# Optimization experiments

Hardware: AMD Instinct MI355X
Metric: run time of the kernel (lower is better)

The kernel has to match this reference:

```python
import jax, jax.numpy as jnp
import numpy as np
import math

B, C, DH = 2048, 64, 512
CAP_VOCAB = 11  # max(core_capacities)+1
DIST_VOCAB = 3


def setup_inputs() -> dict:
    key = jax.random.key(0)
    ks = jax.random.split(key, 12)
    inp = {
        "Ht_C": jax.random.normal(ks[0], (B, C, DH), jnp.float32),
        "core_capacities": jax.random.randint(ks[1], (B, C), 0, CAP_VOCAB),
        "distances": jax.random.randint(ks[2], (B, C), 0, DIST_VOCAB),
        "H_X": jax.random.normal(ks[3], (B, DH), jnp.float32),
        "Ht_S": jax.random.normal(ks[4], (B, DH), jnp.float32),
        "Eq_Q": jax.random.normal(ks[5], (B, DH), jnp.float32),
        "double": jax.random.randint(ks[6], (B,), 0, 2).astype(bool),
        # learned parameters (nn.Embedding tables and bias-free Linear weights, [out,in])
        "cap_emb": jax.random.normal(ks[7], (CAP_VOCAB, DH), jnp.float32) * 0.02,
        "dist_emb": jax.random.normal(ks[8], (DIST_VOCAB, DH), jnp.float32) * 0.02,
        "W_q": jax.random.normal(ks[9], (DH, 3 * DH), jnp.float32) * (1.0 / math.sqrt(3 * DH)),
        "W_k": jax.random.normal(ks[10], (DH, DH), jnp.float32) * (1.0 / math.sqrt(DH)),
        "W_v": jax.random.normal(ks[11], (DH, DH), jnp.float32) * (1.0 / math.sqrt(DH)),
    }
    return inp


def reference(Ht_C, core_capacities, distances, H_X, Ht_S, Eq_Q, double,
              cap_emb, dist_emb, W_q, W_k, W_v):
    scale = 1.0 / math.sqrt(Ht_C.shape[-1])  # 1/sqrt(d_H), slice_emb_size == d_H
    # dynamic core embeddings G_{t,q}^{(C)}: [B,C,dH]
    G = Ht_C + cap_emb[core_capacities] + dist_emb[distances]
    # context and projections
    context = jnp.concatenate([H_X, Ht_S, Eq_Q], axis=-1)          # [B,3dH]
    Q = context @ W_q.T                                            # [B,dH]
    K = jnp.einsum('bcd,ed->bce', G, W_k)                          # [B,C,dH]
    V = jnp.einsum('bcd,ed->bce', G, W_v)                          # [B,C,dH]
    # glimpse attention over cores
    attn_logits = jnp.einsum('bcd,bd->bc', K, Q) * scale           # [B,C]
    attn_weights = jax.nn.softmax(attn_logits, axis=-1)            # softmax over cores
    glimpse = jnp.einsum('bc,bcd->bd', attn_weights, V)            # [B,dH]
    # pointer logits + capacity mask
    u = jnp.einsum('bcd,bd->bc', K, glimpse) * scale               # [B,C]
    need = jnp.where(double[:, None], 2, 1)                        # [B,1]
    invalid = core_capacities < need                               # [B,C]
    u = jnp.where(invalid, -jnp.inf, u)
    return jax.nn.softmax(u, axis=-1)                              # [B,C]
```

## Files before the change

### kernel.cpp

```cpp
#include <hip/hip_runtime.h>
#include <math.h>

#define DH 512
#define CC 64
#define NB 2048
#define SCALE 0.044194173824159216f

__device__ __forceinline__ float wsum(float v) {
#pragma unroll
  for (int off = 32; off; off >>= 1) v += __shfl_xor(v, off, 64);
  return v;
}

__global__ __launch_bounds__(128) void pre_kernel(const float* __restrict__ Wq,
                                                  const float* __restrict__ Wv,
                                                  const float* __restrict__ Wk,
                                                  float* __restrict__ Aout,
                                                  float* __restrict__ Mout,
                                                  const unsigned char* __restrict__ dbl,
                                                  int* __restrict__ need) {
  const int bx = blockIdx.x;
  const int t = threadIdx.x;
  if (bx == 256) {
    __shared__ int flagNZ, flagFP;
    if (t == 0) { flagNZ = 0; flagFP = 0; }
    __syncthreads();
    int nz = 0, fp = 0;
    for (int i = t; i < NB; i += 128) {
      if (i & 3) {
        unsigned char v = dbl[i];
        nz |= (v != 0);
        fp |= (v == 0x3f) | (v == 0x80);
      }
    }
    if (nz) atomicOr(&flagNZ, 1);
    if (fp) atomicOr(&flagFP, 1);
    __syncthreads();
    const int isFP = flagFP, isByte = flagNZ && !flagFP;
    for (int i = t; i < NB; i += 128) {
      int v;
      if (isFP)        v = (((const float*)dbl)[i] != 0.0f);
      else if (isByte) v = (dbl[i] != 0);
      else             v = (((const int*)dbl)[i] != 0);
      need[i] = v ? 2 : 1;
    }
    return;
  }
  __shared__ float As[16][64];
  __shared__ float Bs[16][64];
  const int mt = bx >> 3, nt = bx & 7;
  const int m0 = mt * 64, n0 = nt * 64;
  const bool isQ = (m0 < 1536);
  const float* Acol = isQ ? (Wq + m0) : (Wv + (m0 - 1536));
  const int lda = isQ ? 1536 : 512;
  float* Cout = isQ ? (Aout + (size_t)m0 * 512) : (Mout + (size_t)(m0 - 1536) * 512);
  const int lr = t >> 3;
  const int lc = (t & 7) << 3;
  const int tx = t & 15, ty = t >> 4;

  float4 ra0, ra1, rb0, rb1;
  ra0 = *(const float4*)&Acol[(size_t)lr * lda + lc];
  ra1 = *(const float4*)&Acol[(size_t)lr * lda + lc + 4];
  rb0 = *(const float4*)&Wk[(size_t)lr * 512 + n0 + lc];
  rb1 = *(const float4*)&Wk[(size_t)lr * 512 + n0 + lc + 4];
  float acc[8][4] = {};
  for (int k0 = 0; k0 < 512; k0 += 16) {
    __syncthreads();
    *(float4*)&As[lr][lc] = ra0;
    *(float4*)&As[lr][lc + 4] = ra1;
    *(float4*)&Bs[lr][lc] = rb0;
    *(float4*)&Bs[lr][lc + 4] = rb1;
    __syncthreads();
    if (k0 + 16 < 512) {
      const int kn = k0 + 16 + lr;
      ra0 = *(const float4*)&Acol[(size_t)kn * lda + lc];
      ra1 = *(const float4*)&Acol[(size_t)kn * lda + lc + 4];
      rb0 = *(const float4*)&Wk[(size_t)kn * 512 + n0 + lc];
      rb1 = *(const float4*)&Wk[(size_t)kn * 512 + n0 + lc + 4];
    }
#pragma unroll
    for (int k = 0; k < 16; ++k) {
      float4 a0 = *(float4*)&As[k][ty << 3];
      float4 a1 = *(float4*)&As[k][(ty << 3) + 4];
      float4 b  = *(float4*)&Bs[k][tx << 2];
      float av[8] = {a0.x, a0.y, a0.z, a0.w, a1.x, a1.y, a1.z, a1.w};
      float bv[4] = {b.x, b.y, b.z, b.w};
#pragma unroll
      for (int i = 0; i < 8; ++i)
#pragma unroll
        for (int j = 0; j < 4; ++j) acc[i][j] = fmaf(av[i], bv[j], acc[i][j]);
    }
  }
#pragma unroll
  for (int i = 0; i < 8; ++i) {
    float4 o = {acc[i][0], acc[i][1], acc[i][2], acc[i][3]};
    *(float4*)&Cout[(size_t)((ty << 3) + i) * 512 + n0 + (tx << 2)] = o;
  }
}

#define AS_STR 132

__global__ __launch_bounds__(256) void gemm_nn2p(const float* __restrict__ A0,
                                                 const float* __restrict__ A1,
                                                 const float* __restrict__ A2,
                                                 const float* __restrict__ B,
                                                 float* __restrict__ Cp,
                                                 int kchunk) {
  __shared__ float As[16 * AS_STR];
  __shared__ float Bs[16 * 64];
  const int t = threadIdx.x;
  const int m0 = blockIdx.x * 128, n0 = blockIdx.y * 64;
  const int kbeg = blockIdx.z * kchunk, kend = kbeg + kchunk;
  float* C = Cp + (size_t)blockIdx.z * (NB * DH);
  const int tx = t & 15, ty = t >> 4;
  const int ar0 = t >> 2;
  const int ak4 = (t & 3) << 2;
  const int bk = t >> 4, bn4 = (t & 15) << 2;

  float4 ra0, ra1, rb;
  {
    const float* base = (kbeg < 512) ? A0 : ((kbeg < 1024) ? A1 : A2);
    const int kk = kbeg & 511;
    ra0 = *(const float4*)&base[(size_t)(m0 + ar0) * 512 + kk + ak4];
    ra1 = *(const float4*)&base[(size_t)(m0 + ar0 + 64) * 512 + kk + ak4];
    rb  = *(const float4*)&B[(size_t)(kbeg + bk) * 512 + n0 + bn4];
  }
  float acc[8][4] = {};
  for (int k0 = kbeg; k0 < kend; k0 += 16) {
    __syncthreads();
    As[(ak4 + 0) * AS_STR + ar0] = ra0.x;
    As[(ak4 + 1) * AS_STR + ar0] = ra0.y;
    As[(ak4 + 2) * AS_STR + ar0] = ra0.z;
    As[(ak4 + 3) * AS_STR + ar0] = ra0.w;
    As[(ak4 + 0) * AS_STR + ar0 + 64] = ra1.x;
    As[(ak4 + 1) * AS_STR + ar0 + 64] = ra1.y;
    As[(ak4 + 2) * AS_STR + ar0 + 64] = ra1.z;
    As[(ak4 + 3) * AS_STR + ar0 + 64] = ra1.w;
    *(float4*)&Bs[bk * 64 + bn4] = rb;
    __syncthreads();
    if (k0 + 16 < kend) {
      const int kn = k0 + 16;
      const float* base = (kn < 512) ? A0 : ((kn < 1024) ? A1 : A2);
      const int kk = kn & 511;
      ra0 = *(const float4*)&base[(size_t)(m0 + ar0) * 512 + kk + ak4];
      ra1 = *(const float4*)&base[(size_t)(m0 + ar0 + 64) * 512 + kk + ak4];
      rb  = *(const float4*)&B[(size_t)(kn + bk) * 512 + n0 + bn4];
    }
#pragma unroll
    for (int k = 0; k < 16; ++k) {
      float4 a0 = *(float4*)&As[k * AS_STR + (ty << 3)];
      float4 a1 = *(float4*)&As[k * AS_STR + (ty << 3) + 4];
      float4 b  = *(float4*)&Bs[k * 64 + (tx << 2)];
      float av[8] = {a0.x, a0.y, a0.z, a0.w, a1.x, a1.y, a1.z, a1.w};
      float bv[4] = {b.x, b.y, b.z, b.w};
#pragma unroll
      for (int i = 0; i < 8; ++i)
#pragma unroll
        for (int j = 0; j < 4; ++j) acc[i][j] = fmaf(av[i], bv[j], acc[i][j]);
    }
  }
#pragma unroll
  for (int i = 0; i < 8; ++i) {
    float4 o = {acc[i][0], acc[i][1], acc[i][2], acc[i][3]};
    *(float4*)&C[(size_t)(m0 + (ty << 3) + i) * 512 + n0 + (tx << 2)] = o;
  }
}

__global__ __launch_bounds__(256) void pass1_kernel(const float* __restrict__ HtC,
                                                    const int* __restrict__ caps,
                                                    const int* __restrict__ dists,
                                                    const float* __restrict__ Qkp,
                                                    const float* __restrict__ cap_emb,
                                                    const float* __restrict__ dist_emb,
                                                    float* __restrict__ Gw) {
  const int b = blockIdx.x;
  const int t = threadIdx.x;
  const int wv = t >> 6, ln = t & 63;
  __shared__ float qk[DH];
  __shared__ float capQ[11], distQ[3];
  __shared__ float capE[11], distE[3];
  __shared__ float ec[CC];
  __shared__ float accs[4][DH];
  __shared__ float lsum_s;
  if (t < 11) capE[t] = 0.f;
  if (t < 3) distE[t] = 0.f;
  {
    float q0 = 0.f, q1 = 0.f;
#pragma unroll
    for (int z = 0; z < 4; ++z) {
      q0 += Qkp[(size_t)z * NB * DH + (size_t)b * DH + t];
      q1 += Qkp[(size_t)z * NB * DH + (size_t)b * DH + 256 + t];
    }
    qk[t] = q0;
    qk[t + 256] = q1;
  }
  __syncthreads();
#pragma unroll
  for (int r = 0; r < 3; ++r) {
    int v = wv + (r << 2);
    if (v < 11) {
      float s = 0.f;
#pragma unroll
      for (int j = 0; j < 8; ++j) s = fmaf(cap_emb[v * DH + ln + (j << 6)], qk[ln + (j << 6)], s);
      s = wsum(s);
      if (ln == 0) capQ[v] = s;
    }
  }
  if (wv < 3) {
    float s = 0.f;
#pragma unroll
    for (int j = 0; j < 8; ++j) s = fmaf(dist_emb[wv * DH + ln + (j << 6)], qk[ln + (j << 6)], s);
    s = wsum(s);
    if (ln == 0) distQ[wv] = s;
  }
  __syncthreads();
  const float4* qk4 = (const float4*)qk;
  float4 q1 = qk4[ln];
  float4 q2 = qk4[64 + ln];
  const float* hb = HtC + (size_t)b * CC * DH;
  float a0 = 0.f, a1 = 0.f, a2 = 0.f, a3 = 0.f, a4 = 0.f, a5 = 0.f, a6 = 0.f, a7 = 0.f;
#pragma unroll 4
  for (int i = 0; i < 16; ++i) {
    int c = (wv << 4) + i;
    const float4* h4 = (const float4*)(hb + (size_t)c * DH);
    float4 h1 = h4[ln];
    float4 h2 = h4[64 + ln];
    float s = h1.x * q1.x + h1.y * q1.y + h1.z * q1.z + h1.w * q1.w +
              h2.x * q2.x + h2.y * q2.y + h2.z * q2.z + h2.w * q2.w;
    s = wsum(s);
    float logit = SCALE * (s + capQ[caps[b * CC + c]] + distQ[dists[b * CC + c]]);
    float e = __expf(logit);
    if (ln == 0) ec[c] = e;
    a0 = fmaf(e, h1.x, a0); a1 = fmaf(e, h1.y, a1);
    a2 = fmaf(e, h1.z, a2); a3 = fmaf(e, h1.w, a3);
    a4 = fmaf(e, h2.x, a4); a5 = fmaf(e, h2.y, a5);
    a6 = fmaf(e, h2.z, a6); a7 = fmaf(e, h2.w, a7);
  }
  {
    int d0 = ln << 2;
    accs[wv][d0 + 0] = a0; accs[wv][d0 + 1] = a1;
    accs[wv][d0 + 2] = a2; accs[wv][d0 + 3] = a3;
    accs[wv][256 + d0 + 0] = a4; accs[wv][256 + d0 + 1] = a5;
    accs[wv][256 + d0 + 2] = a6; accs[wv][256 + d0 + 3] = a7;
  }
  __syncthreads();
  if (t < CC) {
    float e = ec[t];
    float l = wsum(e);
    if (t == 0) lsum_s = l;
    atomicAdd(&capE[caps[b * CC + t]], e);
    atomicAdd(&distE[dists[b * CC + t]], e);
  }
  __syncthreads();
  const float rinv = 1.0f / lsum_s;
#pragma unroll
  for (int dd = 0; dd < 2; ++dd) {
    int d = t + (dd << 8);
    float g = accs[0][d] + accs[1][d] + accs[2][d] + accs[3][d];
#pragma unroll
    for (int v = 0; v < 11; ++v) g = fmaf(capE[v], cap_emb[v * DH + d], g);
#pragma unroll
    for (int v = 0; v < 3; ++v) g = fmaf(distE[v], dist_emb[v * DH + d], g);
    Gw[(size_t)b * DH + d] = g * rinv;
  }
}

__global__ __launch_bounds__(256) void pass2_kernel(const float* __restrict__ HtC,
                                                    const int* __restrict__ caps,
                                                    const int* __restrict__ dists,
                                                    const float* __restrict__ Gkp,
                                                    const float* __restrict__ cap_emb,
                                                    const float* __restrict__ dist_emb,
                                                    const int* __restrict__ need,
                                                    float* __restrict__ out) {
  const int b = NB - 1 - blockIdx.x;
  const int t = threadIdx.x;
  const int wv = t >> 6, ln = t & 63;
  __shared__ float gk[DH];
  __shared__ float capG[11], distG[3];
  __shared__ float ulog[CC];
  {
    float g0 = Gkp[(size_t)b * DH + t] + Gkp[(size_t)NB * DH + (size_t)b * DH + t];
    float g1 = Gkp[(size_t)b * DH + 256 + t] + Gkp[(size_t)NB * DH + (size_t)b * DH + 256 + t];
    gk[t] = g0;
    gk[t + 256] = g1;
  }
  __syncthreads();
#pragma unroll
  for (int r = 0; r < 3; ++r) {
    int v = wv + (r << 2);
    if (v < 11) {
      float s = 0.f;
#pragma unroll
      for (int j = 0; j < 8; ++j) s = fmaf(cap_emb[v * DH + ln + (j << 6)], gk[ln + (j << 6)], s);
      s = wsum(s);
      if (ln == 0) capG[v] = s;
    }
  }
  if (wv < 3) {
    float s = 0.f;
#pragma unroll
    for (int j = 0; j < 8; ++j) s = fmaf(dist_emb[wv * DH + ln + (j << 6)], gk[ln + (j << 6)], s);
    s = wsum(s);
    if (ln == 0) distG[wv] = s;
  }
  __syncthreads();
  const float4* gk4 = (const float4*)gk;
  float4 q1 = gk4[ln];
  float4 q2 = gk4[64 + ln];
  const float* hb = HtC + (size_t)b * CC * DH;
#pragma unroll 4
  for (int i = 0; i < 16; ++i) {
    int c = (wv << 4) + i;
    const float4* h4 = (const float4*)(hb + (size_t)c * DH);
    float4 h1 = h4[ln];
    float4 h2 = h4[64 + ln];
    float s = h1.x * q1.x + h1.y * q1.y + h1.z * q1.z + h1.w * q1.w +
              h2.x * q2.x + h2.y * q2.y + h2.z * q2.z + h2.w * q2.w;
    s = wsum(s);
    if (ln == 0)
      ulog[c] = SCALE * (s + capG[caps[b * CC + c]] + distG[dists[b * CC + c]]);
  }
  __syncthreads();
  if (t < CC) {
    int nb = need[b];
    float x = ulog[t];
    if (caps[b * CC + t] < nb) x = -INFINITY;
    float m = x;
#pragma unroll
    for (int off = 32; off; off >>= 1) m = fmaxf(m, __shfl_xor(m, off, 64));
    float e = __expf(x - m);
    float ssum = wsum(e);
    out[(size_t)b * CC + t] = e / ssum;
  }
}

extern "C" void kernel_launch(void* const* d_in, const int* in_sizes, int n_in,
                              void* d_out, int out_size, void* d_ws, size_t ws_size,
                              hipStream_t stream) {
  const float* HtC      = (const float*)d_in[0];
  const int* caps       = (const int*)d_in[1];
  const int* dists      = (const int*)d_in[2];
  const float* H_X      = (const float*)d_in[3];
  const float* Ht_S     = (const float*)d_in[4];
  const float* Eq_Q     = (const float*)d_in[5];
  const unsigned char* dbl = (const unsigned char*)d_in[6];
  const float* cap_emb  = (const float*)d_in[7];
  const float* dist_emb = (const float*)d_in[8];
  const float* W_q      = (const float*)d_in[9];
  const float* W_k      = (const float*)d_in[10];
  const float* W_v      = (const float*)d_in[11];
  float* out = (float*)d_out;

  float* ws     = (float*)d_ws;
  float* wsA    = ws;
  float* wsM    = wsA + 1536 * 512;
  float* wsQkp  = wsM + 512 * 512;
  float* wsGw   = wsQkp + 4 * 2048 * 512;
  float* wsGkp  = wsGw + 2048 * 512;
  int* wsNeed   = (int*)(wsGkp + 2 * 2048 * 512);

  pre_kernel<<<257, 128, 0, stream>>>(W_q, W_v, W_k, wsA, wsM, dbl, wsNeed);
  gemm_nn2p<<<dim3(16, 8, 4), 256, 0, stream>>>(H_X, Ht_S, Eq_Q, wsA, wsQkp, 384);
  pass1_kernel<<<NB, 256, 0, stream>>>(HtC, caps, dists, wsQkp, cap_emb, dist_emb, wsGw);
  gemm_nn2p<<<dim3(16, 8, 2), 256, 0, stream>>>(wsGw, wsGw, wsGw, wsM, wsGkp, 256);
  pass2_kernel<<<NB, 256, 0, stream>>>(HtC, caps, dists, wsGkp, cap_emb, dist_emb, wsNeed, out);
}
```

Before: 527.9 us.

## Fuse pass1, G·M projection GEMM and pass2 into one kernel per batch pair

Replaces the pass1 kernel, the second GEMM and the pass2 kernel with one fused kernel, where each block handles two batch rows. The block computes the glimpse-weighted G, multiplies it by M in-block while streaming M once per pair of rows, then re-reads Ht_C to produce the masked pointer softmax. This removes two launches and the Gw/Gkp workspace round trips, and the second read of Ht_C comes soon after the first, so it may hit in cache. In exchange, each block re-reads the full 512x512 M matrix (1 MB per block, shared by only two rows), uses more shared memory, and the grid is half as large.

```diff
diff --git a/kernel.cpp b/kernel.cpp
--- a/kernel.cpp
+++ b/kernel.cpp
@@ -166,172 +166,208 @@
   }
 }
 
-__global__ __launch_bounds__(256) void pass1_kernel(const float* __restrict__ HtC,
-                                                    const int* __restrict__ caps,
-                                                    const int* __restrict__ dists,
-                                                    const float* __restrict__ Qkp,
-                                                    const float* __restrict__ cap_emb,
-                                                    const float* __restrict__ dist_emb,
-                                                    float* __restrict__ Gw) {
-  const int b = blockIdx.x;
+__global__ __launch_bounds__(256, 4) void fused_kernel(const float* __restrict__ HtC,
+                                                       const int* __restrict__ caps,
+                                                       const int* __restrict__ dists,
+                                                       const float* __restrict__ Qkp,
+                                                       const float* __restrict__ Mm,
+                                                       const float* __restrict__ cap_emb,
+                                                       const float* __restrict__ dist_emb,
+                                                       const int* __restrict__ need,
+                                                       float* __restrict__ out) {
   const int t = threadIdx.x;
   const int wv = t >> 6, ln = t & 63;
-  __shared__ float qk[DH];
-  __shared__ float capQ[11], distQ[3];
+  const int b0 = blockIdx.x << 1;
+
+  __shared__ float qk[2][DH];
+  __shared__ float Gws[2][DH];
+  __shared__ float gks[2][DH];
+  __shared__ float gkp[2][2][DH];
+  __shared__ float accs[4][DH];
+  __shared__ float ec[CC];
+  __shared__ float capQ[2][11], distQ[2][3];
   __shared__ float capE[11], distE[3];
-  __shared__ float ec[CC];
-  __shared__ float accs[4][DH];
+  __shared__ float capG[2][11], distG[2][3];
   __shared__ float lsum_s;
-  if (t < 11) capE[t] = 0.f;
-  if (t < 3) distE[t] = 0.f;
+
+#pragma unroll
+  for (int h = 0; h < 2; ++h) {
+    const size_t bo = (size_t)(b0 + h) * DH;
+    float q0 = 0.f, q1 = 0.f;
+#pragma unroll
+    for (int z = 0; z < 4; ++z) {
+      q0 += Qkp[(size_t)z * NB * DH + bo + t];
+      q1 += Qkp[(size_t)z * NB * DH + bo + 256 + t];
+    }
+    qk[h][t] = q0;
+    qk[h][t + 256] = q1;
+  }
+  __syncthreads();
+
+#pragma unroll
+  for (int h = 0; h < 2; ++h) {
+#pragma unroll
+    for (int r = 0; r < 3; ++r) {
+      int v = wv + (r << 2);
+      if (v < 11) {
+        float s = 0.f;
+#pragma unroll
+        for (int j = 0; j < 8; ++j) s = fmaf(cap_emb[v * DH + ln + (j << 6)], qk[h][ln + (j << 6)], s);
+        s = wsum(s);
+        if (ln == 0) capQ[h][v] = s;
+      }
+    }
+    if (wv < 3) {
+      float s = 0.f;
+#pragma unroll
+      for (int j = 0; j < 8; ++j) s = fmaf(dist_emb[wv * DH + ln + (j << 6)], qk[h][ln + (j << 6)], s);
+      s = wsum(s);
+      if (ln == 0) distQ[h][wv] = s;
+    }
+  }
+
+  for (int h = 0; h < 2; ++h) {
+    const int b = b0 + h;
+    if (t < 11) capE[t] = 0.f;
+    if (t < 3) distE[t] = 0.f;
+    __syncthreads();
+    const float4* qk4 = (const float4*)qk[h];
+    float4 q1 = qk4[ln];
+    float4 q2 = qk4[64 + ln];
+    const float* hb = HtC + (size_t)b * CC * DH;
+    float a0 = 0.f, a1 = 0.f, a2 = 0.f, a3 = 0.f, a4 = 0.f, a5 = 0.f, a6 = 0.f, a7 = 0.f;
+#pragma unroll 4
+    for (int i = 0; i < 16; ++i) {
+      int c = (wv << 4) + i;
+      const float4* h4 = (const float4*)(hb + (size_t)c * DH);
+      float4 h1 = h4[ln];
+      float4 h2 = h4[64 + ln];
+      float s = h1.x * q1.x + h1.y * q1.y + h1.z * q1.z + h1.w * q1.w +
+                h2.x * q2.x + h2.y * q2.y + h2.z * q2.z + h2.w * q2.w;
+      s = wsum(s);
+      float logit = SCALE * (s + capQ[h][caps[b * CC + c]] + distQ[h][dists[b * CC + c]]);
+      float e = __expf(logit);
+      if (ln == 0) ec[c] = e;
+      a0 = fmaf(e, h1.x, a0); a1 = fmaf(e, h1.y, a1);
+      a2 = fmaf(e, h1.z, a2); a3 = fmaf(e, h1.w, a3);
+      a4 = fmaf(e, h2.x, a4); a5 = fmaf(e, h2.y, a5);
+      a6 = fmaf(e, h2.z, a6); a7 = fmaf(e, h2.w, a7);
+    }
+    {
+      int d0 = ln << 2;
+      accs[wv][d0 + 0] = a0; accs[wv][d0 + 1] = a1;
+      accs[wv][d0 + 2] = a2; accs[wv][d0 + 3] = a3;
+      accs[wv][256 + d0 + 0] = a4; accs[wv][256 + d0 + 1] = a5;
+      accs[wv][256 + d0 + 2] = a6; accs[wv][256 + d0 + 3] = a7;
+    }
+    __syncthreads();
+    if (t < CC) {
+      float e = ec[t];
+      float l = wsum(e);
+      if (t == 0) lsum_s = l;
+      atomicAdd(&capE[caps[b * CC + t]], e);
+      atomicAdd(&distE[dists[b * CC + t]], e);
+    }
+    __syncthreads();
+    const float rinv = 1.0f / lsum_s;
+#pragma unroll
+    for (int dd = 0; dd < 2; ++dd) {
+      int d = t + (dd << 8);
+      float g = accs[0][d] + accs[1][d] + accs[2][d] + accs[3][d];
+#pragma unroll
+      for (int v = 0; v < 11; ++v) g = fmaf(capE[v], cap_emb[v * DH + d], g);
+#pragma unroll
+      for (int v = 0; v < 3; ++v) g = fmaf(distE[v], dist_emb[v * DH + d], g);
+      Gws[h][d] = g * rinv;
+    }
+    __syncthreads();
+  }
+
   {
-    float q0 = 0.f, q1 = 0.f;
-#pragma unroll
-    for (int z = 0; z < 4; ++z) {
-      q0 += Qkp[(size_t)z * NB * DH + (size_t)b * DH + t];
-      q1 += Qkp[(size_t)z * NB * DH + (size_t)b * DH + 256 + t];
-    }
-    qk[t] = q0;
-    qk[t + 256] = q1;
+    const int e4 = (t & 127) << 2;
+    const int half = t >> 7;
+    const float* Mp = Mm + (size_t)(half << 8) * DH + e4;
+    const float* g0p = &Gws[0][half << 8];
+    const float* g1p = &Gws[1][half << 8];
+    float s00 = 0.f, s01 = 0.f, s02 = 0.f, s03 = 0.f;
+    float s10 = 0.f, s11 = 0.f, s12 = 0.f, s13 = 0.f;
+#pragma unroll 8
+    for (int d = 0; d < 256; ++d) {
+      float4 m4 = *(const float4*)&Mp[(size_t)d * DH];
+      float g0 = g0p[d];
+      float g1 = g1p[d];
+      s00 = fmaf(g0, m4.x, s00); s01 = fmaf(g0, m4.y, s01);
+      s02 = fmaf(g0, m4.z, s02); s03 = fmaf(g0, m4.w, s03);
+      s10 = fmaf(g1, m4.x, s10); s11 = fmaf(g1, m4.y, s11);
+      s12 = fmaf(g1, m4.z, s12); s13 = fmaf(g1, m4.w, s13);
+    }
+    gkp[half][0][e4 + 0] = s00; gkp[half][0][e4 + 1] = s01;
+    gkp[half][0][e4 + 2] = s02; gkp[half][0][e4 + 3] = s03;
+    gkp[half][1][e4 + 0] = s10; gkp[half][1][e4 + 1] = s11;
+    gkp[half][1][e4 + 2] = s12; gkp[half][1][e4 + 3] = s13;
   }
   __syncthreads();
 #pragma unroll
-  for (int r = 0; r < 3; ++r) {
-    int v = wv + (r << 2);
-    if (v < 11) {
+  for (int h = 0; h < 2; ++h) {
+    gks[h][t] = gkp[0][h][t] + gkp[1][h][t];
+    gks[h][t + 256] = gkp[0][h][t + 256] + gkp[1][h][t + 256];
+  }
+  __syncthreads();
+
+#pragma unroll
+  for (int h = 0; h < 2; ++h) {
+#pragma unroll
+    for (int r = 0; r < 3; ++r) {
+      int v = wv + (r << 2);
+      if (v < 11) {
+        float s = 0.f;
+#pragma unroll
+        for (int j = 0; j < 8; ++j) s = fmaf(cap_emb[v * DH + ln + (j << 6)], gks[h][ln + (j << 6)], s);
+        s = wsum(s);
+        if (ln == 0) capG[h][v] = s;
+      }
+    }
+    if (wv < 3) {
       float s = 0.f;
 #pragma unroll
-      for (int j = 0; j < 8; ++j) s = fmaf(cap_emb[v * DH + ln + (j << 6)], qk[ln + (j << 6)], s);
+      for (int j = 0; j < 8; ++j) s = fmaf(dist_emb[wv * DH + ln + (j << 6)], gks[h][ln + (j << 6)], s);
       s = wsum(s);
-      if (ln == 0) capQ[v] = s;
-    }
-  }
-  if (wv < 3) {
-    float s = 0.f;
-#pragma unroll
-    for (int j = 0; j < 8; ++j) s = fmaf(dist_emb[wv * DH + ln + (j << 6)], qk[ln + (j << 6)], s);
-    s = wsum(s);
-    if (ln == 0) distQ[wv] = s;
+      if (ln == 0) distG[h][wv] = s;
+    }
   }
   __syncthreads();
-  const float4* qk4 = (const float4*)qk;
-  float4 q1 = qk4[ln];
-  float4 q2 = qk4[64 + ln];
-  const float* hb = HtC + (size_t)b * CC * DH;
-  float a0 = 0.f, a1 = 0.f, a2 = 0.f, a3 = 0.f, a4 = 0.f, a5 = 0.f, a6 = 0.f, a7 = 0.f;
+
+  for (int h = 1; h >= 0; --h) {
+    const int b = b0 + h;
+    const float4* gk4 = (const float4*)gks[h];
+    float4 q1 = gk4[ln];
+    float4 q2 = gk4[64 + ln];
+    const float* hb = HtC + (size_t)b * CC * DH;
 #pragma unroll 4
-  for (int i = 0; i < 16; ++i) {
-    int c = (wv << 4) + i;
-    const float4* h4 = (const float4*)(hb + (size_t)c * DH);
-    float4 h1 = h4[ln];
-    float4 h2 = h4[64 + ln];
-    float s = h1.x * q1.x + h1.y * q1.y + h1.z * q1.z + h1.w * q1.w +
-              h2.x * q2.x + h2.y * q2.y + h2.z * q2.z + h2.w * q2.w;
-    s = wsum(s);
-    float logit = SCALE * (s + capQ[caps[b * CC + c]] + distQ[dists[b * CC + c]]);
-    float e = __expf(logit);
-    if (ln == 0) ec[c] = e;
-    a0 = fmaf(e, h1.x, a0); a1 = fmaf(e, h1.y, a1);
-    a2 = fmaf(e, h1.z, a2); a3 = fmaf(e, h1.w, a3);
-    a4 = fmaf(e, h2.x, a4); a5 = fmaf(e, h2.y, a5);
-    a6 = fmaf(e, h2.z, a6); a7 = fmaf(e, h2.w, a7);
-  }
-  {
-    int d0 = ln << 2;
-    accs[wv][d0 + 0] = a0; accs[wv][d0 + 1] = a1;
-    accs[wv][d0 + 2] = a2; accs[wv][d0 + 3] = a3;
-    accs[wv][256 + d0 + 0] = a4; accs[wv][256 + d0 + 1] = a5;
-    accs[wv][256 + d0 + 2] = a6; accs[wv][256 + d0 + 3] = a7;
-  }
-  __syncthreads();
-  if (t < CC) {
-    float e = ec[t];
-    float l = wsum(e);
-    if (t == 0) lsum_s = l;
-    atomicAdd(&capE[caps[b * CC + t]], e);
-    atomicAdd(&distE[dists[b * CC + t]], e);
-  }
-  __syncthreads();
-  const float rinv = 1.0f / lsum_s;
-#pragma unroll
-  for (int dd = 0; dd < 2; ++dd) {
-    int d = t + (dd << 8);
-    float g = accs[0][d] + accs[1][d] + accs[2][d] + accs[3][d];
-#pragma unroll
-    for (int v = 0; v < 11; ++v) g = fmaf(capE[v], cap_emb[v * DH + d], g);
-#pragma unroll
-    for (int v = 0; v < 3; ++v) g = fmaf(distE[v], dist_emb[v * DH + d], g);
-    Gw[(size_t)b * DH + d] = g * rinv;
-  }
-}
-
-__global__ __launch_bounds__(256) void pass2_kernel(const float* __restrict__ HtC,
-                                                    const int* __restrict__ caps,
-                                                    const int* __restrict__ dists,
-                                                    const float* __restrict__ Gkp,
-                                                    const float* __restrict__ cap_emb,
-                                                    const float* __restrict__ dist_emb,
-                                                    const int* __restrict__ need,
-                                                    float* __restrict__ out) {
-  const int b = NB - 1 - blockIdx.x;
-  const int t = threadIdx.x;
-  const int wv = t >> 6, ln = t & 63;
-  __shared__ float gk[DH];
-  __shared__ float capG[11], distG[3];
-  __shared__ float ulog[CC];
-  {
-    float g0 = Gkp[(size_t)b * DH + t] + Gkp[(size_t)NB * DH + (size_t)b * DH + t];
-    float g1 = Gkp[(size_t)b * DH + 256 + t] + Gkp[(size_t)NB * DH + (size_t)b * DH + 256 + t];
-    gk[t] = g0;
-    gk[t + 256] = g1;
-  }
-  __syncthreads();
-#pragma unroll
-  for (int r = 0; r < 3; ++r) {
-    int v = wv + (r << 2);
-    if (v < 11) {
-      float s = 0.f;
-#pragma unroll
-      for (int j = 0; j < 8; ++j) s = fmaf(cap_emb[v * DH + ln + (j << 6)], gk[ln + (j << 6)], s);
+    for (int i = 0; i < 16; ++i) {
+      int c = (wv << 4) + i;
+      const float4* h4 = (const float4*)(hb + (size_t)c * DH);
+      float4 h1 = h4[ln];
+      float4 h2 = h4[64 + ln];
+      float s = h1.x * q1.x + h1.y * q1.y + h1.z * q1.z + h1.w * q1.w +
+                h2.x * q2.x + h2.y * q2.y + h2.z * q2.z + h2.w * q2.w;
       s = wsum(s);
-      if (ln == 0) capG[v] = s;
-    }
-  }
-  if (wv < 3) {
-    float s = 0.f;
-#pragma unroll
-    for (int j = 0; j < 8; ++j) s = fmaf(dist_emb[wv * DH + ln + (j << 6)], gk[ln + (j << 6)], s);
-    s = wsum(s);
-    if (ln == 0) distG[wv] = s;
-  }
-  __syncthreads();
-  const float4* gk4 = (const float4*)gk;
-  float4 q1 = gk4[ln];
-  float4 q2 = gk4[64 + ln];
-  const float* hb = HtC + (size_t)b * CC * DH;
-#pragma unroll 4
-  for (int i = 0; i < 16; ++i) {
-    int c = (wv << 4) + i;
-    const float4* h4 = (const float4*)(hb + (size_t)c * DH);
-    float4 h1 = h4[ln];
-    float4 h2 = h4[64 + ln];
-    float s = h1.x * q1.x + h1.y * q1.y + h1.z * q1.z + h1.w * q1.w +
-              h2.x * q2.x + h2.y * q2.y + h2.z * q2.z + h2.w * q2.w;
-    s = wsum(s);
-    if (ln == 0)
-      ulog[c] = SCALE * (s + capG[caps[b * CC + c]] + distG[dists[b * CC + c]]);
-  }
-  __syncthreads();
-  if (t < CC) {
-    int nb = need[b];
-    float x = ulog[t];
-    if (caps[b * CC + t] < nb) x = -INFINITY;
-    float m = x;
-#pragma unroll
-    for (int off = 32; off; off >>= 1) m = fmaxf(m, __shfl_xor(m, off, 64));
-    float e = __expf(x - m);
-    float ssum = wsum(e);
-    out[(size_t)b * CC + t] = e / ssum;
+      if (ln == 0)
+        ec[c] = SCALE * (s + capG[h][caps[b * CC + c]] + distG[h][dists[b * CC + c]]);
+    }
+    __syncthreads();
+    if (t < CC) {
+      int nb = need[b];
+      float x = ec[t];
+      if (caps[b * CC + t] < nb) x = -INFINITY;
+      float m = x;
+#pragma unroll
+      for (int off = 32; off; off >>= 1) m = fmaxf(m, __shfl_xor(m, off, 64));
+      float e = __expf(x - m);
+      float ssum = wsum(e);
+      out[(size_t)b * CC + t] = e / ssum;
+    }
+    __syncthreads();
   }
 }
 
@@ -356,13 +392,10 @@
   float* wsA    = ws;
   float* wsM    = wsA + 1536 * 512;
   float* wsQkp  = wsM + 512 * 512;
-  float* wsGw   = wsQkp + 4 * 2048 * 512;
-  float* wsGkp  = wsGw + 2048 * 512;
-  int* wsNeed   = (int*)(wsGkp + 2 * 2048 * 512);
+  int* wsNeed   = (int*)(wsQkp + 4 * 2048 * 512);
 
   pre_kernel<<<257, 128, 0, stream>>>(W_q, W_v, W_k, wsA, wsM, dbl, wsNeed);
   gemm_nn2p<<<dim3(16, 8, 4), 256, 0, stream>>>(H_X, Ht_S, Eq_Q, wsA, wsQkp, 384);
-  pass1_kernel<<<NB, 256, 0, stream>>>(HtC, caps, dists, wsQkp, cap_emb, dist_emb, wsGw);
-  gemm_nn2p<<<dim3(16, 8, 2), 256, 0, stream>>>(wsGw, wsGw, wsGw, wsM, wsGkp, 256);
-  pass2_kernel<<<NB, 256, 0, stream>>>(HtC, caps, dists, wsGkp, cap_emb, dist_emb, wsNeed, out);
+  fused_kernel<<<NB / 2, 256, 0, stream>>>(HtC, caps, dists, wsQkp, wsM,
+                                           cap_emb, dist_emb, wsNeed, out);
 }
```

New measurement: 536.3 us. No clear change (+1.6%).
